# Kernel tuning notes

Measured on AMD Instinct MI355X. Metric: run time of the kernel, lower is better.

The kernel has to match this reference:

```python
import jax, jax.numpy as jnp
import numpy as np
import math

EMB_DIM = 1024
N_HEADS = 16
HEAD_DIM = EMB_DIM // N_HEADS
B, T = 4, 2048


def bitlinear(x, w):
    # BitNet b1.58 absmean ternary quantization. NOTE: the source never
    # rescales the ternary weights by `scale`, so forward uses raw {-1,0,1}.
    scale = jnp.maximum(jnp.mean(jnp.abs(w)), 1e-8)
    w_ternary = jnp.clip(jnp.round(w / scale), -1.0, 1.0)
    w_q = w + jax.lax.stop_gradient(w_ternary - w)  # STE
    return x @ w_q.T


def setup_inputs() -> dict:
    key = jax.random.key(0)
    k1, k2, k3 = jax.random.split(key, 3)
    x = jax.random.normal(k1, (B, T, EMB_DIM), dtype=jnp.float32)
    w_qkv = jax.random.normal(k2, (3 * EMB_DIM, EMB_DIM), dtype=jnp.float32) * 0.02
    w_out = jax.random.normal(k3, (EMB_DIM, EMB_DIM), dtype=jnp.float32) * 0.02
    return {"x": x, "w_qkv": w_qkv, "w_out": w_out}


def reference(x, w_qkv, w_out):
    Bc, Tc, C = x.shape
    qkv = bitlinear(x, w_qkv)  # [B, T, 3C]
    q, k, v = jnp.split(qkv, 3, axis=2)

    def split_heads(t):  # [B, T, C] -> [B, H, T, D]
        return t.reshape(Bc, Tc, N_HEADS, HEAD_DIM).transpose(0, 2, 1, 3)

    q, k, v = split_heads(q), split_heads(k), split_heads(v)
    scale = math.sqrt(HEAD_DIM)
    scores = jnp.einsum("bhqd,bhkd->bhqk", q, k) / scale  # [B, H, T, T]
    causal = jnp.triu(jnp.ones((Tc, Tc), dtype=bool), k=1)
    scores = jnp.where(causal, -jnp.inf, scores)
    attn = jax.nn.softmax(scores, axis=-1)
    out = jnp.einsum("bhqk,bhkd->bhqd", attn, v)  # [B, H, T, D]
    out = out.transpose(0, 2, 1, 3).reshape(Bc, Tc, C)
    return bitlinear(out, w_out)
```

## Files before the change

kernel.cpp:

```cpp
#include <hip/hip_runtime.h>
#include <hip/hip_bf16.h>

#define EMB   1024
#define NHEAD 16
#define HDIM  64
#define BSZ   4
#define SEQ   2048
#define MROWS (BSZ*SEQ)
#define NQKV  (3*EMB)

typedef __bf16 bf16;
typedef __bf16 bf16v8 __attribute__((ext_vector_type(8)));
typedef float  f32v4  __attribute__((ext_vector_type(4)));
typedef int    i32v4  __attribute__((ext_vector_type(4)));

#define MFMA16(a,b,c)  __builtin_amdgcn_mfma_f32_16x16x32_bf16((a),(b),(c),0,0,0)
#define MFMAI8(a,b,c)  __builtin_amdgcn_mfma_i32_16x16x64_i8((a),(b),(c),0,0,0)

__device__ __forceinline__ void gload_lds16(const void* g, void* l) {
  __builtin_amdgcn_global_load_lds((const __attribute__((address_space(1))) void*)g,
                                   (__attribute__((address_space(3))) void*)l,
                                   16, 0, 0);
}


__global__ void zero2_kernel(float* p) { p[threadIdx.x] = 0.f; }

__global__ void abs_sum_kernel(const float* __restrict__ w, int n, float* out) {
  float s = 0.f;
  for (int i = blockIdx.x * blockDim.x + threadIdx.x; i < n; i += gridDim.x * blockDim.x)
    s += fabsf(w[i]);
  #pragma unroll
  for (int off = 32; off; off >>= 1) s += __shfl_down(s, off, 64);
  __shared__ float red[4];
  int lane = threadIdx.x & 63, wid = threadIdx.x >> 6;
  if (lane == 0) red[wid] = s;
  __syncthreads();
  if (threadIdx.x == 0) atomicAdd(out, red[0] + red[1] + red[2] + red[3]);
}

__global__ void ternarize_i8_kernel(const float* __restrict__ w, int n,
                                    const float* __restrict__ sum, char* __restrict__ out) {
  int i = blockIdx.x * blockDim.x + threadIdx.x;
  if (i >= n) return;
  float scale = fmaxf(*sum / (float)n, 1e-8f);
  float t = rintf(w[i] / scale);
  t = fmaxf(-1.f, fminf(1.f, t));
  out[i] = (char)(int)t;
}

__global__ void ternarize_bf16_kernel(const float* __restrict__ w, int n,
                                      const float* __restrict__ sum, bf16* __restrict__ out) {
  int i = blockIdx.x * blockDim.x + threadIdx.x;
  if (i >= n) return;
  float scale = fmaxf(*sum / (float)n, 1e-8f);
  float t = rintf(w[i] / scale);
  t = fmaxf(-1.f, fminf(1.f, t));
  out[i] = (bf16)t;
}

__global__ void quant_x_kernel(const float* __restrict__ x, char* __restrict__ p1,
                               char* __restrict__ p2, char* __restrict__ p3, int n) {
  int i = blockIdx.x * blockDim.x + threadIdx.x;
  if (i >= n) return;
  float v = x[i];
  float q1 = fminf(fmaxf(rintf(v * 16.f), -127.f), 127.f);
  float r1 = v - q1 * 0.0625f;
  float q2 = fminf(fmaxf(rintf(r1 * 4096.f), -127.f), 127.f);
  float r2 = r1 - q2 * (1.f / 4096.f);
  float q3 = fminf(fmaxf(rintf(r2 * 524288.f), -127.f), 127.f);
  p1[i] = (char)(int)q1;
  p2[i] = (char)(int)q2;
  p3[i] = (char)(int)q3;
}


__launch_bounds__(256, 2)
__global__ void gemm_qkv_kernel(const char* __restrict__ xq1, const char* __restrict__ xq2,
                                const char* __restrict__ xq3, const char* __restrict__ w8,
                                bf16* __restrict__ qh, bf16* __restrict__ ql,
                                bf16* __restrict__ kh, bf16* __restrict__ kl,
                                bf16* __restrict__ vv) {
  __shared__ __align__(16) char A1[128 * 64];
  __shared__ __align__(16) char A2[128 * 64];
  __shared__ __align__(16) char Bs[128 * 64];
  const int tid = threadIdx.x;
  const int lane = tid & 63, wid = tid >> 6;
  const int quad = lane >> 4, l16 = lane & 15;
  const int m0 = blockIdx.x * 128, n0 = blockIdx.y * 128;
  const int wm = (wid >> 1) * 64, wn = (wid & 1) * 64;
  const int asw = (l16 >> 1) & 3;
  const bool vblk = (n0 >= 2 * EMB);

  float accf[4][4][4];

  {
    i32v4 acc1[4][4] = {};
    i32v4 acc2[4][4] = {};
    for (int kt = 0; kt < EMB / 64; ++kt) {
      __syncthreads();
      #pragma unroll
      for (int r = 0; r < 2; ++r) {
        int li = r * 256 + tid;
        int row = li >> 2, cs = li & 3;
        int cg = cs ^ ((row >> 1) & 3);
        gload_lds16(xq1 + (size_t)(m0 + row) * EMB + kt * 64 + cg * 16, &A1[li * 16]);
        gload_lds16(xq2 + (size_t)(m0 + row) * EMB + kt * 64 + cg * 16, &A2[li * 16]);
        gload_lds16(w8  + (size_t)(n0 + row) * EMB + kt * 64 + cg * 16, &Bs[li * 16]);
      }
      __syncthreads();
      i32v4 af1[4], af2[4], bfr[4];
      #pragma unroll
      for (int i = 0; i < 4; ++i) {
        int off = (wm + i * 16 + l16) * 64 + ((quad ^ asw) * 16);
        af1[i] = *(const i32v4*)&A1[off];
        af2[i] = *(const i32v4*)&A2[off];
        bfr[i] = *(const i32v4*)&Bs[(wn + i * 16 + l16) * 64 + ((quad ^ asw) * 16)];
      }
      #pragma unroll
      for (int i = 0; i < 4; ++i)
        #pragma unroll
        for (int j = 0; j < 4; ++j) {
          acc1[i][j] = MFMAI8(af1[i], bfr[j], acc1[i][j]);
          acc2[i][j] = MFMAI8(af2[i], bfr[j], acc2[i][j]);
        }
    }
    const float S1 = 0.0625f, S2 = 1.f / 4096.f;
    #pragma unroll
    for (int i = 0; i < 4; ++i)
      #pragma unroll
      for (int j = 0; j < 4; ++j)
        #pragma unroll
        for (int r = 0; r < 4; ++r)
          accf[i][j][r] = (float)acc1[i][j][r] * S1 + (float)acc2[i][j][r] * S2;
  }

  if (!vblk) {
    i32v4 acc3[4][4] = {};
    for (int kt = 0; kt < EMB / 64; ++kt) {
      __syncthreads();
      #pragma unroll
      for (int r = 0; r < 2; ++r) {
        int li = r * 256 + tid;
        int row = li >> 2, cs = li & 3;
        int cg = cs ^ ((row >> 1) & 3);
        gload_lds16(xq3 + (size_t)(m0 + row) * EMB + kt * 64 + cg * 16, &A1[li * 16]);
        gload_lds16(w8  + (size_t)(n0 + row) * EMB + kt * 64 + cg * 16, &Bs[li * 16]);
      }
      __syncthreads();
      i32v4 af3[4], bfr[4];
      #pragma unroll
      for (int i = 0; i < 4; ++i) {
        af3[i] = *(const i32v4*)&A1[(wm + i * 16 + l16) * 64 + ((quad ^ asw) * 16)];
        bfr[i] = *(const i32v4*)&Bs[(wn + i * 16 + l16) * 64 + ((quad ^ asw) * 16)];
      }
      #pragma unroll
      for (int i = 0; i < 4; ++i)
        #pragma unroll
        for (int j = 0; j < 4; ++j)
          acc3[i][j] = MFMAI8(af3[i], bfr[j], acc3[i][j]);
    }
    const float S3 = 1.f / 524288.f;
    #pragma unroll
    for (int i = 0; i < 4; ++i)
      #pragma unroll
      for (int j = 0; j < 4; ++j)
        #pragma unroll
        for (int r = 0; r < 4; ++r)
          accf[i][j][r] += (float)acc3[i][j][r] * S3;
  }

  const float QSCALE = 0.18033688011112042f;
  #pragma unroll
  for (int i = 0; i < 4; ++i)
    #pragma unroll
    for (int j = 0; j < 4; ++j)
      #pragma unroll
      for (int r = 0; r < 4; ++r) {
        int m = m0 + wm + i * 16 + quad * 4 + r;
        int n = n0 + wn + j * 16 + l16;
        float c = accf[i][j][r];
        int b = m >> 11, t = m & (SEQ - 1);
        int region = n >> 10, c1 = n & 1023, h = c1 >> 6, d = c1 & 63;
        size_t idx = (((size_t)(b * NHEAD + h) * SEQ + t) << 6) + d;
        if (region == 0)      { float cs = c * QSCALE; bf16 hi = (bf16)cs; qh[idx] = hi; ql[idx] = (bf16)(cs - (float)hi); }
        else if (region == 1) { bf16 hi = (bf16)c; kh[idx] = hi; kl[idx] = (bf16)(c - (float)hi); }
        else                  { vv[idx] = (bf16)c; }
      }
}


__global__ void transpose_v_kernel(const bf16* __restrict__ v, bf16* __restrict__ vt) {
  __shared__ bf16 tile[64 * 72];
  const int tid = threadIdx.x;
  const int bh = blockIdx.y, t0 = blockIdx.x * 64;
  const size_t base = (size_t)bh * SEQ * HDIM;
  #pragma unroll
  for (int r = 0; r < 2; ++r) {
    int li = r * 256 + tid;
    int row = li >> 3, col = (li & 7) * 8;
    bf16v8 val = *(const bf16v8*)(v + base + (size_t)(t0 + row) * HDIM + col);
    #pragma unroll
    for (int j = 0; j < 8; ++j) tile[(col + j) * 72 + row] = val[j];
  }
  __syncthreads();
  #pragma unroll
  for (int r = 0; r < 2; ++r) {
    int li = r * 256 + tid;
    int drow = li >> 3, tcol = (li & 7) * 8;
    bf16v8 val;
    #pragma unroll
    for (int j = 0; j < 8; ++j) val[j] = tile[drow * 72 + tcol + j];
    *(bf16v8*)(vt + base + (size_t)drow * SEQ + t0 + tcol) = val;
  }
}


__launch_bounds__(512, 4)
__global__ void attn_kernel(const bf16* __restrict__ qh, const bf16* __restrict__ ql,
                            const bf16* __restrict__ kh, const bf16* __restrict__ kl,
                            const bf16* __restrict__ vt, bf16* __restrict__ o) {
  __shared__ __align__(16) char smem[66560];
  bf16* Qh = (bf16*)smem;
  bf16* Ql = (bf16*)(smem + 16384);
  bf16* Pw = (bf16*)(smem + 49152);
  const int tid = threadIdx.x;
  const int lane = tid & 63, wid = tid >> 6;
  const int quad = lane >> 4, l16 = lane & 15;
  const int xs = l16 & 7;
  const int pair = blockIdx.x;
  const int bh = blockIdx.y;
  const size_t base = (size_t)bh * SEQ * HDIM;

  const int srow = tid >> 3, scg = (tid & 7) ^ (srow & 7);
  auto stage_kv = [&](char* dst, int k0) {
    gload_lds16(kh + base + (size_t)(k0 + srow) * HDIM + scg * 8, (bf16*)dst + (size_t)tid * 8);
    gload_lds16(kl + base + (size_t)(k0 + srow) * HDIM + scg * 8, (bf16*)(dst + 8192) + (size_t)tid * 8);
    gload_lds16(vt + base + (size_t)srow * SEQ + k0 + scg * 8,    (bf16*)(dst + 16384) + (size_t)tid * 8);
  };

  bf16v8 ones_f;
  {
    bf16 v1 = (l16 == 0) ? (bf16)1.0f : (bf16)0.0f;
    #pragma unroll
    for (int j = 0; j < 8; ++j) ones_f[j] = v1;
  }
  const int b = bh >> 4, h = bh & 15;

  for (int phase = 0; phase < 2; ++phase) {
    const int qt = phase ? (7 - pair) : (8 + pair);
    const int q0 = qt * 128;

    __syncthreads();
    #pragma unroll
    for (int r = 0; r < 2; ++r) {
      int li = r * 512 + tid;
      int row = li >> 3, cg = (li & 7) ^ (row & 7);
      gload_lds16(qh + base + (size_t)(q0 + row) * HDIM + cg * 8, &Qh[li * 8]);
      gload_lds16(ql + base + (size_t)(q0 + row) * HDIM + cg * 8, &Ql[li * 8]);
    }
    __syncthreads();
    bf16v8 qhf[2], qlf[2];
    #pragma unroll
    for (int kk = 0; kk < 2; ++kk) {
      int off = (wid * 16 + l16) * 64 + (((kk << 2) | quad) ^ xs) * 8;
      qhf[kk] = *(const bf16v8*)&Qh[off];
      qlf[kk] = *(const bf16v8*)&Ql[off];
    }
    __syncthreads();

    f32v4 oacc[4] = {};
    f32v4 lacc = {};
    float mrow[4];
    #pragma unroll
    for (int r = 0; r < 4; ++r) mrow[r] = -1e30f;

    const int qrow_hi = q0 + wid * 16 + 15;
    const int ntiles = 2 * qt + 2;

    stage_kv(smem, 0);

    for (int ktile = 0; ktile < ntiles; ++ktile) {
      char* cb = smem + (size_t)((ktile & 1) * 24576);
      char* nb = smem + (size_t)(((ktile + 1) & 1) * 24576);
      __syncthreads();
      if (ktile + 1 < ntiles) stage_kv(nb, (ktile + 1) * 64);
      const int k0 = ktile * 64;
      if (k0 > qrow_hi) continue;

      bf16* Kh_ = (bf16*)cb;
      bf16* Kl_ = (bf16*)(cb + 8192);
      bf16* Vt_ = (bf16*)(cb + 16384);

      f32v4 sacc[4] = {};
      #pragma unroll
      for (int kk = 0; kk < 2; ++kk) {
        const int co = (((kk << 2) | quad) ^ xs) * 8;
        bf16v8 khf[4], klf[4];
        #pragma unroll
        for (int nt = 0; nt < 4; ++nt) {
          khf[nt] = *(const bf16v8*)&Kh_[(nt * 16 + l16) * 64 + co];
          klf[nt] = *(const bf16v8*)&Kl_[(nt * 16 + l16) * 64 + co];
        }
        #pragma unroll
        for (int nt = 0; nt < 4; ++nt) {
          sacc[nt] = MFMA16(qhf[kk], khf[nt], sacc[nt]);
          sacc[nt] = MFMA16(qhf[kk], klf[nt], sacc[nt]);
          sacc[nt] = MFMA16(qlf[kk], khf[nt], sacc[nt]);
        }
      }

      const int qrow_base = q0 + wid * 16 + quad * 4;
      #pragma unroll
      for (int nt = 0; nt < 4; ++nt) {
        int key = k0 + nt * 16 + l16;
        #pragma unroll
        for (int r = 0; r < 4; ++r)
          if (key > qrow_base + r) sacc[nt][r] = -1e30f;
      }
      float mnew[4], alpha[4];
      #pragma unroll
      for (int r = 0; r < 4; ++r) {
        float mx = fmaxf(fmaxf(sacc[0][r], sacc[1][r]), fmaxf(sacc[2][r], sacc[3][r]));
        #pragma unroll
        for (int off = 8; off; off >>= 1) mx = fmaxf(mx, __shfl_xor(mx, off, 64));
        mnew[r] = fmaxf(mrow[r], mx);
        alpha[r] = __builtin_amdgcn_exp2f(mrow[r] - mnew[r]);
        mrow[r] = mnew[r];
      }
      bf16* pwave = Pw + wid * (16 * 68);
      #pragma unroll
      for (int nt = 0; nt < 4; ++nt)
        #pragma unroll
        for (int r = 0; r < 4; ++r)
          pwave[(quad * 4 + r) * 68 + nt * 16 + l16] =
              (bf16)__builtin_amdgcn_exp2f(sacc[nt][r] - mnew[r]);
      #pragma unroll
      for (int r = 0; r < 4; ++r) {
        lacc[r] *= alpha[r];
        #pragma unroll
        for (int dt = 0; dt < 4; ++dt) oacc[dt][r] *= alpha[r];
      }

      #pragma unroll
      for (int kk = 0; kk < 2; ++kk) {
        bf16v8 pf = *(const bf16v8*)&pwave[l16 * 68 + kk * 32 + quad * 8];
        const int co = (((kk << 2) | quad) ^ xs) * 8;
        lacc = MFMA16(pf, ones_f, lacc);
        #pragma unroll
        for (int dt = 0; dt < 4; ++dt) {
          bf16v8 vf = *(const bf16v8*)&Vt_[(dt * 16 + l16) * 64 + co];
          oacc[dt] = MFMA16(pf, vf, oacc[dt]);
        }
      }
    }

    float lrow[4];
    #pragma unroll
    for (int r = 0; r < 4; ++r) lrow[r] = __shfl(lacc[r], lane & 48, 64);

    #pragma unroll
    for (int dt = 0; dt < 4; ++dt)
      #pragma unroll
      for (int r = 0; r < 4; ++r) {
        int q = q0 + wid * 16 + quad * 4 + r;
        int d = dt * 16 + l16;
        float val = oacc[dt][r] / lrow[r];
        o[((size_t)(b * SEQ + q)) * EMB + h * HDIM + d] = (bf16)val;
      }
  }
}


__launch_bounds__(256, 2)
__global__ void gemm_out_kernel(const bf16* __restrict__ oin, const bf16* __restrict__ wt,
                                float* __restrict__ out) {
  __shared__ __align__(16) bf16 As_[128 * 64];
  __shared__ __align__(16) bf16 Bs_[128 * 64];
  const int tid = threadIdx.x;
  const int lane = tid & 63, wid = tid >> 6;
  const int quad = lane >> 4, l16 = lane & 15;
  const int m0 = blockIdx.x * 128, n0 = blockIdx.y * 128;
  const int wm = (wid >> 1) * 64, wn = (wid & 1) * 64;
  f32v4 acc[4][4] = {};

  for (int kt = 0; kt < EMB / 64; ++kt) {
    __syncthreads();
    #pragma unroll
    for (int r = 0; r < 4; ++r) {
      int li = r * 256 + tid;
      int row = li >> 3, col = (li & 7) * 8;
      gload_lds16(oin + (size_t)(m0 + row) * EMB + kt * 64 + col, &As_[li * 8]);
      gload_lds16(wt  + (size_t)(n0 + row) * EMB + kt * 64 + col, &Bs_[li * 8]);
    }
    __syncthreads();
    #pragma unroll
    for (int kk = 0; kk < 2; ++kk) {
      bf16v8 af[4], bfr[4];
      #pragma unroll
      for (int i = 0; i < 4; ++i) {
        af[i]  = *(const bf16v8*)&As_[(wm + i * 16 + l16) * 64 + kk * 32 + quad * 8];
        bfr[i] = *(const bf16v8*)&Bs_[(wn + i * 16 + l16) * 64 + kk * 32 + quad * 8];
      }
      #pragma unroll
      for (int i = 0; i < 4; ++i)
        #pragma unroll
        for (int j = 0; j < 4; ++j)
          acc[i][j] = MFMA16(af[i], bfr[j], acc[i][j]);
    }
  }
  #pragma unroll
  for (int i = 0; i < 4; ++i)
    #pragma unroll
    for (int j = 0; j < 4; ++j)
      #pragma unroll
      for (int r = 0; r < 4; ++r) {
        int m = m0 + wm + i * 16 + quad * 4 + r;
        int n = n0 + wn + j * 16 + l16;
        out[(size_t)m * EMB + n] = acc[i][j][r];
      }
}


extern "C" void kernel_launch(void* const* d_in, const int* in_sizes, int n_in,
                              void* d_out, int out_size, void* d_ws, size_t ws_size,
                              hipStream_t stream) {
  const float* x     = (const float*)d_in[0];
  const float* w_qkv = (const float*)d_in[1];
  const float* w_out = (const float*)d_in[2];
  float* out = (float*)d_out;
  char* ws = (char*)d_ws;

  const size_t SZ  = (size_t)MROWS * EMB * sizeof(bf16);
  const size_t SZ8 = (size_t)MROWS * EMB;
  size_t off = 0;
  float* sums = (float*)ws;            off = 256;
  char*  wq8  = (char*)(ws + off);     off += (size_t)NQKV * EMB;
  bf16*  wo_t = (bf16*)(ws + off);     off += (size_t)EMB * EMB * sizeof(bf16);
  char*  xq1  = (char*)(ws + off);     off += SZ8;
  char*  xq2  = (char*)(ws + off);     off += SZ8;
  char*  xq3  = (char*)(ws + off);     off += SZ8;
  bf16*  qh   = (bf16*)(ws + off);     off += SZ;
  bf16*  ql   = (bf16*)(ws + off);     off += SZ;
  bf16*  kh   = (bf16*)(ws + off);     off += SZ;
  bf16*  kl   = (bf16*)(ws + off);     off += SZ;
  bf16*  vv   = (bf16*)(ws + off);     off += SZ;
  bf16*  vt   = (bf16*)xq1;
  bf16*  ob   = vv;
  (void)in_sizes; (void)n_in; (void)out_size; (void)ws_size;

  zero2_kernel<<<1, 2, 0, stream>>>(sums);
  abs_sum_kernel<<<256, 256, 0, stream>>>(w_qkv, NQKV * EMB, &sums[0]);
  abs_sum_kernel<<<256, 256, 0, stream>>>(w_out, EMB * EMB, &sums[1]);
  ternarize_i8_kernel<<<(NQKV * EMB) / 256, 256, 0, stream>>>(w_qkv, NQKV * EMB, &sums[0], wq8);
  ternarize_bf16_kernel<<<(EMB * EMB) / 256, 256, 0, stream>>>(w_out, EMB * EMB, &sums[1], wo_t);
  quant_x_kernel<<<(MROWS * EMB) / 256, 256, 0, stream>>>(x, xq1, xq2, xq3, MROWS * EMB);
  gemm_qkv_kernel<<<dim3(MROWS / 128, NQKV / 128), 256, 0, stream>>>(xq1, xq2, xq3, wq8, qh, ql, kh, kl, vv);
  transpose_v_kernel<<<dim3(SEQ / 64, BSZ * NHEAD), 256, 0, stream>>>(vv, vt);
  attn_kernel<<<dim3(8, BSZ * NHEAD), 512, 0, stream>>>(qh, ql, kh, kl, vt, ob);
  gemm_out_kernel<<<dim3(MROWS / 128, EMB / 128), 256, 0, stream>>>(ob, wo_t, out);
}
```

Baseline: 378.6 us.

## Fuse prep kernels, double-buffer QKV GEMM, write V transposed, skip unneeded masking

The two abs-sum launches become one, and the weight-ternarize and x-quantize launches become a single prep kernel. The QKV GEMM now double-buffers its LDS stages so the next tile's global-to-LDS load overlaps the current tile's MFMAs, and it drops one barrier per iteration. V blocks write straight into the transposed layout with packed 4-element stores, which removes the separate transpose kernel and its extra pass over memory. The attention kernel applies the causal mask only on tiles that cross the diagonal. The costs are more LDS per block, which may reduce occupancy, and strided transposed stores for V.

```diff
diff --git a/kernel.cpp b/kernel.cpp
--- a/kernel.cpp
+++ b/kernel.cpp
@@ -10,6 +10,7 @@
 #define NQKV  (3*EMB)
 
 typedef __bf16 bf16;
+typedef __bf16 bf16v4 __attribute__((ext_vector_type(4)));
 typedef __bf16 bf16v8 __attribute__((ext_vector_type(8)));
 typedef float  f32v4  __attribute__((ext_vector_type(4)));
 typedef int    i32v4  __attribute__((ext_vector_type(4)));
@@ -26,52 +27,50 @@
 
 __global__ void zero2_kernel(float* p) { p[threadIdx.x] = 0.f; }
 
-__global__ void abs_sum_kernel(const float* __restrict__ w, int n, float* out) {
+__global__ void abs_sum2_kernel(const float* __restrict__ w1, int n1,
+                                const float* __restrict__ w2, int n2, float* out) {
+  const float* w; int n, bid, nblk; float* o;
+  if (blockIdx.x < 256) { w = w1; n = n1; bid = blockIdx.x;       nblk = 256; o = out; }
+  else                  { w = w2; n = n2; bid = blockIdx.x - 256; nblk = 64;  o = out + 1; }
   float s = 0.f;
-  for (int i = blockIdx.x * blockDim.x + threadIdx.x; i < n; i += gridDim.x * blockDim.x)
-    s += fabsf(w[i]);
+  for (int i = bid * 256 + threadIdx.x; i < n; i += nblk * 256) s += fabsf(w[i]);
   #pragma unroll
   for (int off = 32; off; off >>= 1) s += __shfl_down(s, off, 64);
   __shared__ float red[4];
   int lane = threadIdx.x & 63, wid = threadIdx.x >> 6;
   if (lane == 0) red[wid] = s;
   __syncthreads();
-  if (threadIdx.x == 0) atomicAdd(out, red[0] + red[1] + red[2] + red[3]);
-}
-
-__global__ void ternarize_i8_kernel(const float* __restrict__ w, int n,
-                                    const float* __restrict__ sum, char* __restrict__ out) {
-  int i = blockIdx.x * blockDim.x + threadIdx.x;
-  if (i >= n) return;
-  float scale = fmaxf(*sum / (float)n, 1e-8f);
-  float t = rintf(w[i] / scale);
-  t = fmaxf(-1.f, fminf(1.f, t));
-  out[i] = (char)(int)t;
-}
-
-__global__ void ternarize_bf16_kernel(const float* __restrict__ w, int n,
-                                      const float* __restrict__ sum, bf16* __restrict__ out) {
-  int i = blockIdx.x * blockDim.x + threadIdx.x;
-  if (i >= n) return;
-  float scale = fmaxf(*sum / (float)n, 1e-8f);
-  float t = rintf(w[i] / scale);
-  t = fmaxf(-1.f, fminf(1.f, t));
-  out[i] = (bf16)t;
-}
-
-__global__ void quant_x_kernel(const float* __restrict__ x, char* __restrict__ p1,
-                               char* __restrict__ p2, char* __restrict__ p3, int n) {
-  int i = blockIdx.x * blockDim.x + threadIdx.x;
-  if (i >= n) return;
-  float v = x[i];
-  float q1 = fminf(fmaxf(rintf(v * 16.f), -127.f), 127.f);
-  float r1 = v - q1 * 0.0625f;
-  float q2 = fminf(fmaxf(rintf(r1 * 4096.f), -127.f), 127.f);
-  float r2 = r1 - q2 * (1.f / 4096.f);
-  float q3 = fminf(fmaxf(rintf(r2 * 524288.f), -127.f), 127.f);
-  p1[i] = (char)(int)q1;
-  p2[i] = (char)(int)q2;
-  p3[i] = (char)(int)q3;
+  if (threadIdx.x == 0) atomicAdd(o, red[0] + red[1] + red[2] + red[3]);
+}
+
+__global__ void prep_kernel(const float* __restrict__ wq, const float* __restrict__ wo,
+                            const float* __restrict__ x, const float* __restrict__ sums,
+                            char* __restrict__ wq8, bf16* __restrict__ wo_t,
+                            char* __restrict__ p1, char* __restrict__ p2,
+                            char* __restrict__ p3) {
+  const int NW1 = NQKV * EMB, NW2 = EMB * EMB;
+  int gid = blockIdx.x * 256 + threadIdx.x;
+  if (gid < NW1) {
+    float scale = fmaxf(sums[0] / (float)NW1, 1e-8f);
+    float t = rintf(wq[gid] / scale);
+    wq8[gid] = (char)(int)fmaxf(-1.f, fminf(1.f, t));
+  } else if (gid < NW1 + NW2) {
+    int i = gid - NW1;
+    float scale = fmaxf(sums[1] / (float)NW2, 1e-8f);
+    float t = rintf(wo[i] / scale);
+    wo_t[i] = (bf16)fmaxf(-1.f, fminf(1.f, t));
+  } else {
+    int i = gid - NW1 - NW2;
+    float v = x[i];
+    float q1 = fminf(fmaxf(rintf(v * 16.f), -127.f), 127.f);
+    float r1 = v - q1 * 0.0625f;
+    float q2 = fminf(fmaxf(rintf(r1 * 4096.f), -127.f), 127.f);
+    float r2 = r1 - q2 * (1.f / 4096.f);
+    float q3 = fminf(fmaxf(rintf(r2 * 524288.f), -127.f), 127.f);
+    p1[i] = (char)(int)q1;
+    p2[i] = (char)(int)q2;
+    p3[i] = (char)(int)q3;
+  }
 }
 
 
@@ -80,10 +79,8 @@
                                 const char* __restrict__ xq3, const char* __restrict__ w8,
                                 bf16* __restrict__ qh, bf16* __restrict__ ql,
                                 bf16* __restrict__ kh, bf16* __restrict__ kl,
-                                bf16* __restrict__ vv) {
-  __shared__ __align__(16) char A1[128 * 64];
-  __shared__ __align__(16) char A2[128 * 64];
-  __shared__ __align__(16) char Bs[128 * 64];
+                                bf16* __restrict__ vt) {
+  __shared__ __align__(16) char smem[49152];
   const int tid = threadIdx.x;
   const int lane = tid & 63, wid = tid >> 6;
   const int quad = lane >> 4, l16 = lane & 15;
@@ -92,67 +89,78 @@
   const int asw = (l16 >> 1) & 3;
   const bool vblk = (n0 >= 2 * EMB);
 
+  auto stage1 = [&](char* dst, int kt) {
+    #pragma unroll
+    for (int r = 0; r < 2; ++r) {
+      int li = r * 256 + tid;
+      int row = li >> 2, cs = li & 3;
+      int cg = cs ^ ((row >> 1) & 3);
+      gload_lds16(xq1 + (size_t)(m0 + row) * EMB + kt * 64 + cg * 16, dst + li * 16);
+      gload_lds16(xq2 + (size_t)(m0 + row) * EMB + kt * 64 + cg * 16, dst + 8192 + li * 16);
+      gload_lds16(w8  + (size_t)(n0 + row) * EMB + kt * 64 + cg * 16, dst + 16384 + li * 16);
+    }
+  };
+
   float accf[4][4][4];
 
   {
     i32v4 acc1[4][4] = {};
     i32v4 acc2[4][4] = {};
+    stage1(smem, 0);
     for (int kt = 0; kt < EMB / 64; ++kt) {
+      char* cb = smem + (size_t)((kt & 1) * 24576);
+      char* nb = smem + (size_t)(((kt + 1) & 1) * 24576);
       __syncthreads();
+      if (kt + 1 < EMB / 64) stage1(nb, kt + 1);
+      i32v4 af1[4], af2[4], bfr[4];
+      #pragma unroll
+      for (int i = 0; i < 4; ++i) {
+        int off = (wm + i * 16 + l16) * 64 + ((quad ^ asw) * 16);
+        af1[i] = *(const i32v4*)(cb + off);
+        af2[i] = *(const i32v4*)(cb + 8192 + off);
+        bfr[i] = *(const i32v4*)(cb + 16384 + (wn + i * 16 + l16) * 64 + ((quad ^ asw) * 16));
+      }
+      #pragma unroll
+      for (int i = 0; i < 4; ++i)
+        #pragma unroll
+        for (int j = 0; j < 4; ++j) {
+          acc1[i][j] = MFMAI8(af1[i], bfr[j], acc1[i][j]);
+          acc2[i][j] = MFMAI8(af2[i], bfr[j], acc2[i][j]);
+        }
+    }
+    const float S1 = 0.0625f, S2 = 1.f / 4096.f;
+    #pragma unroll
+    for (int i = 0; i < 4; ++i)
+      #pragma unroll
+      for (int j = 0; j < 4; ++j)
+        #pragma unroll
+        for (int r = 0; r < 4; ++r)
+          accf[i][j][r] = (float)acc1[i][j][r] * S1 + (float)acc2[i][j][r] * S2;
+  }
+
+  if (!vblk) {
+    auto stage2 = [&](char* dst, int kt) {
       #pragma unroll
       for (int r = 0; r < 2; ++r) {
         int li = r * 256 + tid;
         int row = li >> 2, cs = li & 3;
         int cg = cs ^ ((row >> 1) & 3);
-        gload_lds16(xq1 + (size_t)(m0 + row) * EMB + kt * 64 + cg * 16, &A1[li * 16]);
-        gload_lds16(xq2 + (size_t)(m0 + row) * EMB + kt * 64 + cg * 16, &A2[li * 16]);
-        gload_lds16(w8  + (size_t)(n0 + row) * EMB + kt * 64 + cg * 16, &Bs[li * 16]);
-      }
+        gload_lds16(xq3 + (size_t)(m0 + row) * EMB + kt * 64 + cg * 16, dst + li * 16);
+        gload_lds16(w8  + (size_t)(n0 + row) * EMB + kt * 64 + cg * 16, dst + 8192 + li * 16);
+      }
+    };
+    i32v4 acc3[4][4] = {};
+    stage2(smem, 0);
+    for (int kt = 0; kt < EMB / 64; ++kt) {
+      char* cb = smem + (size_t)((kt & 1) * 16384);
+      char* nb = smem + (size_t)(((kt + 1) & 1) * 16384);
       __syncthreads();
-      i32v4 af1[4], af2[4], bfr[4];
+      if (kt + 1 < EMB / 64) stage2(nb, kt + 1);
+      i32v4 af3[4], bfr[4];
       #pragma unroll
       for (int i = 0; i < 4; ++i) {
-        int off = (wm + i * 16 + l16) * 64 + ((quad ^ asw) * 16);
-        af1[i] = *(const i32v4*)&A1[off];
-        af2[i] = *(const i32v4*)&A2[off];
-        bfr[i] = *(const i32v4*)&Bs[(wn + i * 16 + l16) * 64 + ((quad ^ asw) * 16)];
-      }
-      #pragma unroll
-      for (int i = 0; i < 4; ++i)
-        #pragma unroll
-        for (int j = 0; j < 4; ++j) {
-          acc1[i][j] = MFMAI8(af1[i], bfr[j], acc1[i][j]);
-          acc2[i][j] = MFMAI8(af2[i], bfr[j], acc2[i][j]);
-        }
-    }
-    const float S1 = 0.0625f, S2 = 1.f / 4096.f;
-    #pragma unroll
-    for (int i = 0; i < 4; ++i)
-      #pragma unroll
-      for (int j = 0; j < 4; ++j)
-        #pragma unroll
-        for (int r = 0; r < 4; ++r)
-          accf[i][j][r] = (float)acc1[i][j][r] * S1 + (float)acc2[i][j][r] * S2;
-  }
-
-  if (!vblk) {
-    i32v4 acc3[4][4] = {};
-    for (int kt = 0; kt < EMB / 64; ++kt) {
-      __syncthreads();
-      #pragma unroll
-      for (int r = 0; r < 2; ++r) {
-        int li = r * 256 + tid;
-        int row = li >> 2, cs = li & 3;
-        int cg = cs ^ ((row >> 1) & 3);
-        gload_lds16(xq3 + (size_t)(m0 + row) * EMB + kt * 64 + cg * 16, &A1[li * 16]);
-        gload_lds16(w8  + (size_t)(n0 + row) * EMB + kt * 64 + cg * 16, &Bs[li * 16]);
-      }
-      __syncthreads();
-      i32v4 af3[4], bfr[4];
-      #pragma unroll
-      for (int i = 0; i < 4; ++i) {
-        af3[i] = *(const i32v4*)&A1[(wm + i * 16 + l16) * 64 + ((quad ^ asw) * 16)];
-        bfr[i] = *(const i32v4*)&Bs[(wn + i * 16 + l16) * 64 + ((quad ^ asw) * 16)];
+        af3[i] = *(const i32v4*)(cb + (wm + i * 16 + l16) * 64 + ((quad ^ asw) * 16));
+        bfr[i] = *(const i32v4*)(cb + 8192 + (wn + i * 16 + l16) * 64 + ((quad ^ asw) * 16));
       }
       #pragma unroll
       for (int i = 0; i < 4; ++i)
@@ -168,50 +176,38 @@
         #pragma unroll
         for (int r = 0; r < 4; ++r)
           accf[i][j][r] += (float)acc3[i][j][r] * S3;
-  }
-
-  const float QSCALE = 0.18033688011112042f;
-  #pragma unroll
-  for (int i = 0; i < 4; ++i)
-    #pragma unroll
-    for (int j = 0; j < 4; ++j)
-      #pragma unroll
-      for (int r = 0; r < 4; ++r) {
-        int m = m0 + wm + i * 16 + quad * 4 + r;
+
+    const float QSCALE = 0.18033688011112042f;
+    const bool qreg = (n0 < EMB);
+    #pragma unroll
+    for (int i = 0; i < 4; ++i)
+      #pragma unroll
+      for (int j = 0; j < 4; ++j)
+        #pragma unroll
+        for (int r = 0; r < 4; ++r) {
+          int m = m0 + wm + i * 16 + quad * 4 + r;
+          int n = n0 + wn + j * 16 + l16;
+          float c = accf[i][j][r];
+          int b = m >> 11, t = m & (SEQ - 1);
+          int c1 = n & 1023, h = c1 >> 6, d = c1 & 63;
+          size_t idx = (((size_t)(b * NHEAD + h) * SEQ + t) << 6) + d;
+          if (qreg) { float cs = c * QSCALE; bf16 hi = (bf16)cs; qh[idx] = hi; ql[idx] = (bf16)(cs - (float)hi); }
+          else      { bf16 hi = (bf16)c;  kh[idx] = hi; kl[idx] = (bf16)(c - (float)hi); }
+        }
+  } else {
+    #pragma unroll
+    for (int i = 0; i < 4; ++i)
+      #pragma unroll
+      for (int j = 0; j < 4; ++j) {
+        int m = m0 + wm + i * 16 + quad * 4;
         int n = n0 + wn + j * 16 + l16;
-        float c = accf[i][j][r];
         int b = m >> 11, t = m & (SEQ - 1);
-        int region = n >> 10, c1 = n & 1023, h = c1 >> 6, d = c1 & 63;
-        size_t idx = (((size_t)(b * NHEAD + h) * SEQ + t) << 6) + d;
-        if (region == 0)      { float cs = c * QSCALE; bf16 hi = (bf16)cs; qh[idx] = hi; ql[idx] = (bf16)(cs - (float)hi); }
-        else if (region == 1) { bf16 hi = (bf16)c; kh[idx] = hi; kl[idx] = (bf16)(c - (float)hi); }
-        else                  { vv[idx] = (bf16)c; }
-      }
-}
-
-
-__global__ void transpose_v_kernel(const bf16* __restrict__ v, bf16* __restrict__ vt) {
-  __shared__ bf16 tile[64 * 72];
-  const int tid = threadIdx.x;
-  const int bh = blockIdx.y, t0 = blockIdx.x * 64;
-  const size_t base = (size_t)bh * SEQ * HDIM;
-  #pragma unroll
-  for (int r = 0; r < 2; ++r) {
-    int li = r * 256 + tid;
-    int row = li >> 3, col = (li & 7) * 8;
-    bf16v8 val = *(const bf16v8*)(v + base + (size_t)(t0 + row) * HDIM + col);
-    #pragma unroll
-    for (int j = 0; j < 8; ++j) tile[(col + j) * 72 + row] = val[j];
-  }
-  __syncthreads();
-  #pragma unroll
-  for (int r = 0; r < 2; ++r) {
-    int li = r * 256 + tid;
-    int drow = li >> 3, tcol = (li & 7) * 8;
-    bf16v8 val;
-    #pragma unroll
-    for (int j = 0; j < 8; ++j) val[j] = tile[drow * 72 + tcol + j];
-    *(bf16v8*)(vt + base + (size_t)drow * SEQ + t0 + tcol) = val;
+        int c1 = n & 1023, h = c1 >> 6, d = c1 & 63;
+        bf16v4 pack;
+        #pragma unroll
+        for (int r = 0; r < 4; ++r) pack[r] = (bf16)accf[i][j][r];
+        *(bf16v4*)(vt + ((size_t)(b * NHEAD + h) * HDIM + d) * SEQ + t) = pack;
+      }
   }
 }
 
@@ -275,7 +271,8 @@
     #pragma unroll
     for (int r = 0; r < 4; ++r) mrow[r] = -1e30f;
 
-    const int qrow_hi = q0 + wid * 16 + 15;
+    const int qrow_lo = q0 + wid * 16;
+    const int qrow_hi = qrow_lo + 15;
     const int ntiles = 2 * qt + 2;
 
     stage_kv(smem, 0);
@@ -310,13 +307,15 @@
         }
       }
 
-      const int qrow_base = q0 + wid * 16 + quad * 4;
-      #pragma unroll
-      for (int nt = 0; nt < 4; ++nt) {
-        int key = k0 + nt * 16 + l16;
-        #pragma unroll
-        for (int r = 0; r < 4; ++r)
-          if (key > qrow_base + r) sacc[nt][r] = -1e30f;
+      if (k0 + 63 > qrow_lo) {
+        const int qrow_base = q0 + wid * 16 + quad * 4;
+        #pragma unroll
+        for (int nt = 0; nt < 4; ++nt) {
+          int key = k0 + nt * 16 + l16;
+          #pragma unroll
+          for (int r = 0; r < 4; ++r)
+            if (key > qrow_base + r) sacc[nt][r] = -1e30f;
+        }
       }
       float mnew[4], alpha[4];
       #pragma unroll
@@ -444,19 +443,16 @@
   bf16*  ql   = (bf16*)(ws + off);     off += SZ;
   bf16*  kh   = (bf16*)(ws + off);     off += SZ;
   bf16*  kl   = (bf16*)(ws + off);     off += SZ;
-  bf16*  vv   = (bf16*)(ws + off);     off += SZ;
-  bf16*  vt   = (bf16*)xq1;
-  bf16*  ob   = vv;
+  bf16*  vt   = (bf16*)(ws + off);     off += SZ;
+  bf16*  ob   = (bf16*)xq1;
   (void)in_sizes; (void)n_in; (void)out_size; (void)ws_size;
 
   zero2_kernel<<<1, 2, 0, stream>>>(sums);
-  abs_sum_kernel<<<256, 256, 0, stream>>>(w_qkv, NQKV * EMB, &sums[0]);
-  abs_sum_kernel<<<256, 256, 0, stream>>>(w_out, EMB * EMB, &sums[1]);
-  ternarize_i8_kernel<<<(NQKV * EMB) / 256, 256, 0, stream>>>(w_qkv, NQKV * EMB, &sums[0], wq8);
-  ternarize_bf16_kernel<<<(EMB * EMB) / 256, 256, 0, stream>>>(w_out, EMB * EMB, &sums[1], wo_t);
-  quant_x_kernel<<<(MROWS * EMB) / 256, 256, 0, stream>>>(x, xq1, xq2, xq3, MROWS * EMB);
-  gemm_qkv_kernel<<<dim3(MROWS / 128, NQKV / 128), 256, 0, stream>>>(xq1, xq2, xq3, wq8, qh, ql, kh, kl, vv);
-  transpose_v_kernel<<<dim3(SEQ / 64, BSZ * NHEAD), 256, 0, stream>>>(vv, vt);
+  abs_sum2_kernel<<<320, 256, 0, stream>>>(w_qkv, NQKV * EMB, w_out, EMB * EMB, sums);
+  prep_kernel<<<(NQKV * EMB + EMB * EMB + MROWS * EMB) / 256, 256, 0, stream>>>(
+      w_qkv, w_out, x, sums, wq8, wo_t, xq1, xq2, xq3);
+  gemm_qkv_kernel<<<dim3(MROWS / 128, NQKV / 128), 256, 0, stream>>>(
+      xq1, xq2, xq3, wq8, qh, ql, kh, kl, vt);
   attn_kernel<<<dim3(8, BSZ * NHEAD), 512, 0, stream>>>(qh, ql, kh, kl, vt, ob);
   gemm_out_kernel<<<dim3(MROWS / 128, EMB / 128), 256, 0, stream>>>(ob, wo_t, out);
 }
```

Result: no change. 372.0 us (-1.7%).
